# Kernel tuning notes

Measured on AMD Instinct MI355X. Metric: run time of the kernel, lower is better.

## Reference

```python
import jax, jax.numpy as jnp
import numpy as np

C = 6.5  # ALCOVE specificity constant

BATCH, NE, NDIMS = 2048, 2048, 128


def setup_inputs() -> dict:
    key = jax.random.key(0)
    k1, k2, k3 = jax.random.split(key, 3)
    inputs = jax.random.normal(k1, (BATCH, NDIMS), dtype=jnp.float32)
    exemplars = jax.random.normal(k2, (NE, NDIMS), dtype=jnp.float32)
    # attn initialized to ones/ndims in the original; use positive random values
    # scaled similarly so the exp argument stays in a reasonable range.
    attn = jax.random.uniform(k3, (NDIMS,), dtype=jnp.float32) / float(NDIMS)
    return {"inputs": inputs, "exemplars": exemplars, "attn": attn}


def reference(inputs, exemplars, attn):
    # Vectorized form of: exp(-c * sum_d attn_d * |exemplars - x|) per example.
    # diff: (batch, ne, ndims)
    diff = jnp.abs(exemplars[None, :, :] - inputs[:, None, :])
    dist = jnp.einsum('bed,d->be', diff, attn)  # weighted L1 distance
    return jnp.exp(-C * dist)  # (batch, ne)
```

## Files before the change

kernel.cpp:

```cpp
#include <hip/hip_runtime.h>
#include <stdint.h>


#define BATCH 2048
#define NE 2048
#define ND 128

#define TB 64
#define TE 64
#define KC 64

#define QSCALE 16777216.0f
#define QBIAS  2097152.5f
#define KEXP   (-6.5f / 16777216.0f)

#define SAD(acc, a, b) asm("v_sad_u32 %0, %1, %2, %0" : "+v"(acc) : "v"(a), "v"(b))

__global__ __launch_bounds__(256, 4)
void alcove_rbf_kernel(const float* __restrict__ X,
                       const float* __restrict__ E,
                       const float* __restrict__ A,
                       float* __restrict__ out) {
  __shared__ uint32_t Xs[KC * TB];
  __shared__ uint32_t Es[KC * TE];

  const int tid = threadIdx.x;
  const int e0 = blockIdx.x * TE;
  const int b0 = blockIdx.y * TB;

  const int tx = tid & 15;
  const int ty = tid >> 4;
  const int lane_in = tid & 3;

  uint32_t acc[4][4];
#pragma unroll
  for (int j = 0; j < 4; ++j)
#pragma unroll
    for (int i = 0; i < 4; ++i) acc[j][i] = 0u;

  for (int kc = 0; kc < ND; kc += KC) {
    if (kc) __syncthreads();

    const float4* A4 = reinterpret_cast<const float4*>(A + kc);

#pragma unroll
    for (int it = 0; it < 4; ++it) {
      int g = it * 64 + (tid >> 2);
      int row = g & (TB - 1);
      int c4 = 4 * (g >> 6) + lane_in;
      float4 a = A4[c4];
      float4 as;
      as.x = a.x * QSCALE; as.y = a.y * QSCALE;
      as.z = a.z * QSCALE; as.w = a.w * QSCALE;
      int dbase = 4 * c4;

      float4 vx = reinterpret_cast<const float4*>(X + (size_t)(b0 + row) * ND + kc)[c4];
      Xs[(dbase + 0) * TB + row] = (uint32_t)fmaf(vx.x, as.x, QBIAS);
      Xs[(dbase + 1) * TB + row] = (uint32_t)fmaf(vx.y, as.y, QBIAS);
      Xs[(dbase + 2) * TB + row] = (uint32_t)fmaf(vx.z, as.z, QBIAS);
      Xs[(dbase + 3) * TB + row] = (uint32_t)fmaf(vx.w, as.w, QBIAS);

      float4 ve = reinterpret_cast<const float4*>(E + (size_t)(e0 + row) * ND + kc)[c4];
      Es[(dbase + 0) * TE + row] = (uint32_t)fmaf(ve.x, as.x, QBIAS);
      Es[(dbase + 1) * TE + row] = (uint32_t)fmaf(ve.y, as.y, QBIAS);
      Es[(dbase + 2) * TE + row] = (uint32_t)fmaf(ve.z, as.z, QBIAS);
      Es[(dbase + 3) * TE + row] = (uint32_t)fmaf(ve.w, as.w, QBIAS);
    }
    __syncthreads();

    const uint4* Xs4 = reinterpret_cast<const uint4*>(Xs);
    const uint4* Es4 = reinterpret_cast<const uint4*>(Es);
#pragma unroll 4
    for (int d = 0; d < KC; ++d) {
      uint4 xv = Xs4[d * (TB / 4) + ty];
      uint4 ev = Es4[d * (TE / 4) + tx];
      SAD(acc[0][0], xv.x, ev.x); SAD(acc[0][1], xv.x, ev.y);
      SAD(acc[0][2], xv.x, ev.z); SAD(acc[0][3], xv.x, ev.w);
      SAD(acc[1][0], xv.y, ev.x); SAD(acc[1][1], xv.y, ev.y);
      SAD(acc[1][2], xv.y, ev.z); SAD(acc[1][3], xv.y, ev.w);
      SAD(acc[2][0], xv.z, ev.x); SAD(acc[2][1], xv.z, ev.y);
      SAD(acc[2][2], xv.z, ev.z); SAD(acc[2][3], xv.z, ev.w);
      SAD(acc[3][0], xv.w, ev.x); SAD(acc[3][1], xv.w, ev.y);
      SAD(acc[3][2], xv.w, ev.z); SAD(acc[3][3], xv.w, ev.w);
    }
  }

#pragma unroll
  for (int j = 0; j < 4; ++j) {
    int b = b0 + 4 * ty + j;
    float4 o;
    o.x = __expf(KEXP * (float)acc[j][0]);
    o.y = __expf(KEXP * (float)acc[j][1]);
    o.z = __expf(KEXP * (float)acc[j][2]);
    o.w = __expf(KEXP * (float)acc[j][3]);
    reinterpret_cast<float4*>(out + (size_t)b * NE + e0)[tx] = o;
  }
}

extern "C" void kernel_launch(void* const* d_in, const int* in_sizes, int n_in,
                              void* d_out, int out_size, void* d_ws, size_t ws_size,
                              hipStream_t stream) {
  const float* X = (const float*)d_in[0];
  const float* E = (const float*)d_in[1];
  const float* A = (const float*)d_in[2];
  float* out = (float*)d_out;

  dim3 grid(NE / TE, BATCH / TB);
  dim3 block(256);
  alcove_rbf_kernel<<<grid, block, 0, stream>>>(X, E, A, out);
}
```

Before: 81.94 us.

## Retile to 32x256 blocks with 8x4 per-thread SAD tile and register prefetch

Changes the block tile from 64x64 to 32 batch rows by 256 exemplars and the per-thread tile from 4x4 to 8x4, so each exemplar LDS read feeds 32 SADs and the X values are broadcast across the wave. The exemplar LDS array gets a padded stride, and the next K-chunk's global loads go into registers while the current chunk is computed. The aim is to cut LDS traffic per SAD and hide global-load latency. In exchange, register pressure rises (launch bounds drop to 2 blocks per SIMD), and there are more but smaller K chunks with more barriers.

```diff
diff --git a/kernel.cpp b/kernel.cpp
--- a/kernel.cpp
+++ b/kernel.cpp
@@ -6,9 +6,11 @@
 #define NE 2048
 #define ND 128
 
-#define TB 64
-#define TE 64
-#define KC 64
+#define TB 32
+#define TE 256
+#define KC 32
+#define SE 260
+#define NCHUNK (ND / KC)
 
 #define QSCALE 16777216.0f
 #define QBIAS  2097152.5f
@@ -16,84 +18,106 @@
 
 #define SAD(acc, a, b) asm("v_sad_u32 %0, %1, %2, %0" : "+v"(acc) : "v"(a), "v"(b))
 
-__global__ __launch_bounds__(256, 4)
+__global__ __launch_bounds__(256, 2)
 void alcove_rbf_kernel(const float* __restrict__ X,
                        const float* __restrict__ E,
                        const float* __restrict__ A,
                        float* __restrict__ out) {
-  __shared__ uint32_t Xs[KC * TB];
-  __shared__ uint32_t Es[KC * TE];
+  __shared__ __align__(16) uint32_t Es[KC * SE];
+  __shared__ __align__(16) uint32_t Xs[KC * TB];
 
   const int tid = threadIdx.x;
+  const int lane = tid & 63;
+  const int w = tid >> 6;
   const int e0 = blockIdx.x * TE;
   const int b0 = blockIdx.y * TB;
 
-  const int tx = tid & 15;
-  const int ty = tid >> 4;
-  const int lane_in = tid & 3;
+  const int c4 = tid & 7;
+  const int srow = tid >> 3;
 
-  uint32_t acc[4][4];
+  uint32_t acc[8][4];
 #pragma unroll
-  for (int j = 0; j < 4; ++j)
+  for (int j = 0; j < 8; ++j)
 #pragma unroll
     for (int i = 0; i < 4; ++i) acc[j][i] = 0u;
 
-  for (int kc = 0; kc < ND; kc += KC) {
-    if (kc) __syncthreads();
+  float4 eP[8], xP, aP;
+  {
+    aP = reinterpret_cast<const float4*>(A)[c4];
+#pragma unroll
+    for (int it = 0; it < 8; ++it)
+      eP[it] = reinterpret_cast<const float4*>(
+                   E + (size_t)(e0 + it * 32 + srow) * ND)[c4];
+    xP = reinterpret_cast<const float4*>(X + (size_t)(b0 + srow) * ND)[c4];
+  }
 
-    const float4* A4 = reinterpret_cast<const float4*>(A + kc);
+#pragma unroll 1
+  for (int c = 0; c < NCHUNK; ++c) {
+    if (c) __syncthreads();
 
+    float4 as;
+    as.x = aP.x * QSCALE; as.y = aP.y * QSCALE;
+    as.z = aP.z * QSCALE; as.w = aP.w * QSCALE;
+    const int dbase = 4 * c4;
 #pragma unroll
-    for (int it = 0; it < 4; ++it) {
-      int g = it * 64 + (tid >> 2);
-      int row = g & (TB - 1);
-      int c4 = 4 * (g >> 6) + lane_in;
-      float4 a = A4[c4];
-      float4 as;
-      as.x = a.x * QSCALE; as.y = a.y * QSCALE;
-      as.z = a.z * QSCALE; as.w = a.w * QSCALE;
-      int dbase = 4 * c4;
-
-      float4 vx = reinterpret_cast<const float4*>(X + (size_t)(b0 + row) * ND + kc)[c4];
-      Xs[(dbase + 0) * TB + row] = (uint32_t)fmaf(vx.x, as.x, QBIAS);
-      Xs[(dbase + 1) * TB + row] = (uint32_t)fmaf(vx.y, as.y, QBIAS);
-      Xs[(dbase + 2) * TB + row] = (uint32_t)fmaf(vx.z, as.z, QBIAS);
-      Xs[(dbase + 3) * TB + row] = (uint32_t)fmaf(vx.w, as.w, QBIAS);
-
-      float4 ve = reinterpret_cast<const float4*>(E + (size_t)(e0 + row) * ND + kc)[c4];
-      Es[(dbase + 0) * TE + row] = (uint32_t)fmaf(ve.x, as.x, QBIAS);
-      Es[(dbase + 1) * TE + row] = (uint32_t)fmaf(ve.y, as.y, QBIAS);
-      Es[(dbase + 2) * TE + row] = (uint32_t)fmaf(ve.z, as.z, QBIAS);
-      Es[(dbase + 3) * TE + row] = (uint32_t)fmaf(ve.w, as.w, QBIAS);
+    for (int it = 0; it < 8; ++it) {
+      int row = it * 32 + srow;
+      Es[(dbase + 0) * SE + row] = (uint32_t)fmaf(eP[it].x, as.x, QBIAS);
+      Es[(dbase + 1) * SE + row] = (uint32_t)fmaf(eP[it].y, as.y, QBIAS);
+      Es[(dbase + 2) * SE + row] = (uint32_t)fmaf(eP[it].z, as.z, QBIAS);
+      Es[(dbase + 3) * SE + row] = (uint32_t)fmaf(eP[it].w, as.w, QBIAS);
     }
+    Xs[(dbase + 0) * TB + srow] = (uint32_t)fmaf(xP.x, as.x, QBIAS);
+    Xs[(dbase + 1) * TB + srow] = (uint32_t)fmaf(xP.y, as.y, QBIAS);
+    Xs[(dbase + 2) * TB + srow] = (uint32_t)fmaf(xP.z, as.z, QBIAS);
+    Xs[(dbase + 3) * TB + srow] = (uint32_t)fmaf(xP.w, as.w, QBIAS);
     __syncthreads();
 
+    if (c + 1 < NCHUNK) {
+      const int kn = (c + 1) * KC;
+      aP = reinterpret_cast<const float4*>(A + kn)[c4];
+#pragma unroll
+      for (int it = 0; it < 8; ++it)
+        eP[it] = reinterpret_cast<const float4*>(
+                     E + (size_t)(e0 + it * 32 + srow) * ND + kn)[c4];
+      xP = reinterpret_cast<const float4*>(X + (size_t)(b0 + srow) * ND + kn)[c4];
+    }
+
+    const uint4* Es4 = reinterpret_cast<const uint4*>(Es);
     const uint4* Xs4 = reinterpret_cast<const uint4*>(Xs);
-    const uint4* Es4 = reinterpret_cast<const uint4*>(Es);
-#pragma unroll 4
+#pragma unroll 8
     for (int d = 0; d < KC; ++d) {
-      uint4 xv = Xs4[d * (TB / 4) + ty];
-      uint4 ev = Es4[d * (TE / 4) + tx];
-      SAD(acc[0][0], xv.x, ev.x); SAD(acc[0][1], xv.x, ev.y);
-      SAD(acc[0][2], xv.x, ev.z); SAD(acc[0][3], xv.x, ev.w);
-      SAD(acc[1][0], xv.y, ev.x); SAD(acc[1][1], xv.y, ev.y);
-      SAD(acc[1][2], xv.y, ev.z); SAD(acc[1][3], xv.y, ev.w);
-      SAD(acc[2][0], xv.z, ev.x); SAD(acc[2][1], xv.z, ev.y);
-      SAD(acc[2][2], xv.z, ev.z); SAD(acc[2][3], xv.z, ev.w);
-      SAD(acc[3][0], xv.w, ev.x); SAD(acc[3][1], xv.w, ev.y);
-      SAD(acc[3][2], xv.w, ev.z); SAD(acc[3][3], xv.w, ev.w);
+      uint4 ev = Es4[d * (SE / 4) + lane];
+      uint4 xa = Xs4[d * (TB / 4) + 2 * w];
+      uint4 xb = Xs4[d * (TB / 4) + 2 * w + 1];
+      SAD(acc[0][0], xa.x, ev.x); SAD(acc[0][1], xa.x, ev.y);
+      SAD(acc[0][2], xa.x, ev.z); SAD(acc[0][3], xa.x, ev.w);
+      SAD(acc[1][0], xa.y, ev.x); SAD(acc[1][1], xa.y, ev.y);
+      SAD(acc[1][2], xa.y, ev.z); SAD(acc[1][3], xa.y, ev.w);
+      SAD(acc[2][0], xa.z, ev.x); SAD(acc[2][1], xa.z, ev.y);
+      SAD(acc[2][2], xa.z, ev.z); SAD(acc[2][3], xa.z, ev.w);
+      SAD(acc[3][0], xa.w, ev.x); SAD(acc[3][1], xa.w, ev.y);
+      SAD(acc[3][2], xa.w, ev.z); SAD(acc[3][3], xa.w, ev.w);
+      SAD(acc[4][0], xb.x, ev.x); SAD(acc[4][1], xb.x, ev.y);
+      SAD(acc[4][2], xb.x, ev.z); SAD(acc[4][3], xb.x, ev.w);
+      SAD(acc[5][0], xb.y, ev.x); SAD(acc[5][1], xb.y, ev.y);
+      SAD(acc[5][2], xb.y, ev.z); SAD(acc[5][3], xb.y, ev.w);
+      SAD(acc[6][0], xb.z, ev.x); SAD(acc[6][1], xb.z, ev.y);
+      SAD(acc[6][2], xb.z, ev.z); SAD(acc[6][3], xb.z, ev.w);
+      SAD(acc[7][0], xb.w, ev.x); SAD(acc[7][1], xb.w, ev.y);
+      SAD(acc[7][2], xb.w, ev.z); SAD(acc[7][3], xb.w, ev.w);
     }
   }
 
 #pragma unroll
-  for (int j = 0; j < 4; ++j) {
-    int b = b0 + 4 * ty + j;
+  for (int j = 0; j < 8; ++j) {
+    int b = b0 + 8 * w + j;
     float4 o;
     o.x = __expf(KEXP * (float)acc[j][0]);
     o.y = __expf(KEXP * (float)acc[j][1]);
     o.z = __expf(KEXP * (float)acc[j][2]);
     o.w = __expf(KEXP * (float)acc[j][3]);
-    reinterpret_cast<float4*>(out + (size_t)b * NE + e0)[tx] = o;
+    reinterpret_cast<float4*>(out + (size_t)b * NE + e0)[lane] = o;
   }
 }
 
```

Result: slower. 86.05 us (+5.0%).

## Switch weighted L1 accumulation to packed fp16 add/abs with single-stage staging

Applied to the files above, without the earlier changes.

Replaces the 32-bit fixed-point v_sad_u32 accumulation with packed fp16 arithmetic. Each uint32 now holds two weighted dimensions, so each inner-loop step covers two dimensions at the cost of a packed subtract, a mask for the absolute value, and a packed add. The whole 128-dim tile is staged into shared memory in one pass with one barrier instead of two chunks. The two fp16 lanes are summed in fp32 before the exp. The cost is reduced precision: fp16 accumulators of weighted distances may exceed the tolerance.

```diff
diff --git a/kernel.cpp b/kernel.cpp
--- a/kernel.cpp
+++ b/kernel.cpp
@@ -1,36 +1,70 @@
 #include <hip/hip_runtime.h>
+#include <hip/hip_fp16.h>
 #include <stdint.h>
 
 
-#define BATCH 2048
-#define NE 2048
 #define ND 128
+#define NEC 2048
+#define CCONST 6.5f
 
-#define TB 64
-#define TE 64
-#define KC 64
+#define AAH(acc, x, e)                                              \
+  {                                                                 \
+    uint32_t t_;                                                    \
+    asm("v_pk_add_f16 %0, %1, %2 neg_lo:[0,1] neg_hi:[0,1]"         \
+        : "=v"(t_) : "v"(x), "v"(e));                               \
+    t_ &= 0x7fff7fffu;                                              \
+    asm("v_pk_add_f16 %0, %0, %1" : "+v"(acc) : "v"(t_));           \
+  }
 
-#define QSCALE 16777216.0f
-#define QBIAS  2097152.5f
-#define KEXP   (-6.5f / 16777216.0f)
+static __device__ __forceinline__ uint32_t pkh(float lo, float hi) {
+  __half2 h = __floats2half2_rn(lo, hi);
+  union { __half2 h; uint32_t u; } cv;
+  cv.h = h;
+  return cv.u;
+}
 
-#define SAD(acc, a, b) asm("v_sad_u32 %0, %1, %2, %0" : "+v"(acc) : "v"(a), "v"(b))
+static __device__ __forceinline__ float hsum(uint32_t u) {
+  union { uint32_t u; __half2 h; } cv;
+  cv.u = u;
+  return __half2float(__low2half(cv.h)) + __half2float(__high2half(cv.h));
+}
 
 __global__ __launch_bounds__(256, 4)
 void alcove_rbf_kernel(const float* __restrict__ X,
                        const float* __restrict__ E,
                        const float* __restrict__ A,
                        float* __restrict__ out) {
-  __shared__ uint32_t Xs[KC * TB];
-  __shared__ uint32_t Es[KC * TE];
+  __shared__ uint32_t Eh[64 * 64];
+  __shared__ uint32_t Xh[64 * 64];
 
   const int tid = threadIdx.x;
-  const int e0 = blockIdx.x * TE;
-  const int b0 = blockIdx.y * TB;
+  const int e0 = blockIdx.x * 64;
+  const int b0 = blockIdx.y * 64;
 
-  const int tx = tid & 15;
-  const int ty = tid >> 4;
-  const int lane_in = tid & 3;
+  {
+    const int r = tid & 63;
+    const int g = tid >> 6;
+    const float4* Ap = reinterpret_cast<const float4*>(A + 32 * g);
+    const float4* Ep = reinterpret_cast<const float4*>(E + (size_t)(e0 + r) * ND + 32 * g);
+    const float4* Xp = reinterpret_cast<const float4*>(X + (size_t)(b0 + r) * ND + 32 * g);
+#pragma unroll
+    for (int k = 0; k < 8; ++k) {
+      float4 a = Ap[k];
+      float4 ev = Ep[k];
+      float4 xv = Xp[k];
+      int dd = 16 * g + 2 * k;
+      Eh[dd * 64 + r]       = pkh(ev.x * a.x, ev.y * a.y);
+      Eh[(dd + 1) * 64 + r] = pkh(ev.z * a.z, ev.w * a.w);
+      Xh[dd * 64 + r]       = pkh(xv.x * a.x, xv.y * a.y);
+      Xh[(dd + 1) * 64 + r] = pkh(xv.z * a.z, xv.w * a.w);
+    }
+  }
+  __syncthreads();
+
+  const int lane = tid & 63;
+  const int w = tid >> 6;
+  const int el = lane & 15;
+  const int xg = lane >> 4;
 
   uint32_t acc[4][4];
 #pragma unroll
@@ -38,62 +72,33 @@
 #pragma unroll
     for (int i = 0; i < 4; ++i) acc[j][i] = 0u;
 
-  for (int kc = 0; kc < ND; kc += KC) {
-    if (kc) __syncthreads();
+  const uint4* Ev = reinterpret_cast<const uint4*>(Eh);
+  const uint4* Xv = reinterpret_cast<const uint4*>(Xh);
+  const int xoff = 4 * w + xg;
 
-    const float4* A4 = reinterpret_cast<const float4*>(A + kc);
-
-#pragma unroll
-    for (int it = 0; it < 4; ++it) {
-      int g = it * 64 + (tid >> 2);
-      int row = g & (TB - 1);
-      int c4 = 4 * (g >> 6) + lane_in;
-      float4 a = A4[c4];
-      float4 as;
-      as.x = a.x * QSCALE; as.y = a.y * QSCALE;
-      as.z = a.z * QSCALE; as.w = a.w * QSCALE;
-      int dbase = 4 * c4;
-
-      float4 vx = reinterpret_cast<const float4*>(X + (size_t)(b0 + row) * ND + kc)[c4];
-      Xs[(dbase + 0) * TB + row] = (uint32_t)fmaf(vx.x, as.x, QBIAS);
-      Xs[(dbase + 1) * TB + row] = (uint32_t)fmaf(vx.y, as.y, QBIAS);
-      Xs[(dbase + 2) * TB + row] = (uint32_t)fmaf(vx.z, as.z, QBIAS);
-      Xs[(dbase + 3) * TB + row] = (uint32_t)fmaf(vx.w, as.w, QBIAS);
-
-      float4 ve = reinterpret_cast<const float4*>(E + (size_t)(e0 + row) * ND + kc)[c4];
-      Es[(dbase + 0) * TE + row] = (uint32_t)fmaf(ve.x, as.x, QBIAS);
-      Es[(dbase + 1) * TE + row] = (uint32_t)fmaf(ve.y, as.y, QBIAS);
-      Es[(dbase + 2) * TE + row] = (uint32_t)fmaf(ve.z, as.z, QBIAS);
-      Es[(dbase + 3) * TE + row] = (uint32_t)fmaf(ve.w, as.w, QBIAS);
-    }
-    __syncthreads();
-
-    const uint4* Xs4 = reinterpret_cast<const uint4*>(Xs);
-    const uint4* Es4 = reinterpret_cast<const uint4*>(Es);
-#pragma unroll 4
-    for (int d = 0; d < KC; ++d) {
-      uint4 xv = Xs4[d * (TB / 4) + ty];
-      uint4 ev = Es4[d * (TE / 4) + tx];
-      SAD(acc[0][0], xv.x, ev.x); SAD(acc[0][1], xv.x, ev.y);
-      SAD(acc[0][2], xv.x, ev.z); SAD(acc[0][3], xv.x, ev.w);
-      SAD(acc[1][0], xv.y, ev.x); SAD(acc[1][1], xv.y, ev.y);
-      SAD(acc[1][2], xv.y, ev.z); SAD(acc[1][3], xv.y, ev.w);
-      SAD(acc[2][0], xv.z, ev.x); SAD(acc[2][1], xv.z, ev.y);
-      SAD(acc[2][2], xv.z, ev.z); SAD(acc[2][3], xv.z, ev.w);
-      SAD(acc[3][0], xv.w, ev.x); SAD(acc[3][1], xv.w, ev.y);
-      SAD(acc[3][2], xv.w, ev.z); SAD(acc[3][3], xv.w, ev.w);
-    }
+#pragma unroll 8
+  for (int dd = 0; dd < 64; ++dd) {
+    uint4 ev = Ev[dd * 16 + el];
+    uint4 xv = Xv[dd * 16 + xoff];
+    AAH(acc[0][0], xv.x, ev.x); AAH(acc[0][1], xv.x, ev.y);
+    AAH(acc[0][2], xv.x, ev.z); AAH(acc[0][3], xv.x, ev.w);
+    AAH(acc[1][0], xv.y, ev.x); AAH(acc[1][1], xv.y, ev.y);
+    AAH(acc[1][2], xv.y, ev.z); AAH(acc[1][3], xv.y, ev.w);
+    AAH(acc[2][0], xv.z, ev.x); AAH(acc[2][1], xv.z, ev.y);
+    AAH(acc[2][2], xv.z, ev.z); AAH(acc[2][3], xv.z, ev.w);
+    AAH(acc[3][0], xv.w, ev.x); AAH(acc[3][1], xv.w, ev.y);
+    AAH(acc[3][2], xv.w, ev.z); AAH(acc[3][3], xv.w, ev.w);
   }
 
 #pragma unroll
   for (int j = 0; j < 4; ++j) {
-    int b = b0 + 4 * ty + j;
+    int b = b0 + 16 * w + 4 * xg + j;
     float4 o;
-    o.x = __expf(KEXP * (float)acc[j][0]);
-    o.y = __expf(KEXP * (float)acc[j][1]);
-    o.z = __expf(KEXP * (float)acc[j][2]);
-    o.w = __expf(KEXP * (float)acc[j][3]);
-    reinterpret_cast<float4*>(out + (size_t)b * NE + e0)[tx] = o;
+    o.x = __expf(-CCONST * hsum(acc[j][0]));
+    o.y = __expf(-CCONST * hsum(acc[j][1]));
+    o.z = __expf(-CCONST * hsum(acc[j][2]));
+    o.w = __expf(-CCONST * hsum(acc[j][3]));
+    reinterpret_cast<float4*>(out + (size_t)b * NEC + e0)[el] = o;
   }
 }
 
@@ -105,7 +110,7 @@
   const float* A = (const float*)d_in[2];
   float* out = (float*)d_out;
 
-  dim3 grid(NE / TE, BATCH / TB);
+  dim3 grid(NEC / 64, 2048 / 64);
   dim3 block(256);
   alcove_rbf_kernel<<<grid, block, 0, stream>>>(X, E, A, out);
 }
```

New measurement: 91.37 us. +11.5%, slower.
